# Optimization experiments

Measured on AMD Instinct MI355X. Metric: run time of the kernel, lower is better.

Reference implementation:

```python
import jax, jax.numpy as jnp
import numpy as np

EMBED = 1024
HEADS = 16
HEAD_DIM = EMBED // HEADS
FF = 4096
EPS = 1e-5


def layer_norm(x, g, b):
    mu = jnp.mean(x, axis=-1, keepdims=True)
    var = jnp.mean(jnp.square(x - mu), axis=-1, keepdims=True)
    return (x - mu) * jax.lax.rsqrt(var + EPS) * g + b


def setup_inputs() -> dict:
    key = jax.random.key(0)
    ks = jax.random.split(key, 16)
    s = 0.02
    x = jax.random.normal(ks[0], (4, 2048, EMBED), dtype=jnp.float32)
    d = {
        "x": x,
        "Wq": jax.random.normal(ks[1], (EMBED, EMBED), jnp.float32) * s,
        "bq": jnp.zeros((EMBED,), jnp.float32),
        "Wk": jax.random.normal(ks[2], (EMBED, EMBED), jnp.float32) * s,
        "bk": jnp.zeros((EMBED,), jnp.float32),
        "Wv": jax.random.normal(ks[3], (EMBED, EMBED), jnp.float32) * s,
        "bv": jnp.zeros((EMBED,), jnp.float32),
        "Wo": jax.random.normal(ks[4], (EMBED, EMBED), jnp.float32) * s,
        "bo": jnp.zeros((EMBED,), jnp.float32),
        "W1": jax.random.normal(ks[5], (EMBED, FF), jnp.float32) * s,
        "b1": jnp.zeros((FF,), jnp.float32),
        "W2": jax.random.normal(ks[6], (FF, EMBED), jnp.float32) * s,
        "b2": jnp.zeros((EMBED,), jnp.float32),
        "ln1_g": jnp.ones((EMBED,), jnp.float32),
        "ln1_b": jnp.zeros((EMBED,), jnp.float32),
        "ln2_g": jnp.ones((EMBED,), jnp.float32),
        "ln2_b": jnp.zeros((EMBED,), jnp.float32),
    }
    return d


def reference(x, Wq, bq, Wk, bk, Wv, bv, Wo, bo, W1, b1, W2, b2, ln1_g, ln1_b, ln2_g, ln2_b):
    B, S, E = x.shape
    scale = np.sqrt(HEAD_DIM).astype(np.float32)
    # project and split heads: (B, H, S, Dh)
    def heads(t):
        return t.reshape(B, S, HEADS, HEAD_DIM).transpose(0, 2, 1, 3)
    Q = heads(x @ Wq + bq)
    K = heads(x @ Wk + bk)
    V = heads(x @ Wv + bv)
    scores = jnp.einsum("bhqd,bhkd->bhqk", Q, K) / scale
    attn = jax.nn.softmax(scores, axis=-1)
    ctx = jnp.einsum("bhqk,bhkd->bhqd", attn, V)
    ctx = ctx.transpose(0, 2, 1, 3).reshape(B, S, E)
    attn_out = ctx @ Wo + bo
    x = layer_norm(x + attn_out, ln1_g, ln1_b)
    ff = jax.nn.relu(x @ W1 + b1) @ W2 + b2
    x = layer_norm(x + ff, ln2_g, ln2_b)
    return x
```

## Files before the change

kernel.cpp:

```cpp
#include <hip/hip_runtime.h>
#include <stdint.h>

typedef uint16_t u16;
typedef __bf16 bf16x8 __attribute__((ext_vector_type(8)));
typedef float f32x4 __attribute__((ext_vector_type(4)));

__device__ __forceinline__ float bf2f(u16 u) {
  union { uint32_t i; float f; } v; v.i = ((uint32_t)u) << 16; return v.f;
}
__device__ __forceinline__ u16 f2bf(float f) {
  union { float f; uint32_t i; } v; v.f = f;
  uint32_t r = v.i + 0x7fffu + ((v.i >> 16) & 1u);
  return (u16)(r >> 16);
}
__device__ __forceinline__ uint32_t pack2(float a, float b) {
  return (uint32_t)f2bf(a) | ((uint32_t)f2bf(b) << 16);
}
__device__ __forceinline__ void gll16(const u16* g, u16* l) {
  __builtin_amdgcn_global_load_lds((const __attribute__((address_space(1))) void*)g,
                                   (__attribute__((address_space(3))) void*)l, 16, 0, 0);
}

__global__ __launch_bounds__(256) void f32_to_bf16(
    const float* __restrict__ in, u16* __restrict__ out)
{
  int idx = blockIdx.x * 256 + threadIdx.x;
  float4 v = *(const float4*)(in + (size_t)idx * 4);
  uint2 o;
  o.x = pack2(v.x, v.y);
  o.y = pack2(v.z, v.w);
  *(uint2*)(out + (size_t)idx * 4) = o;
}

__global__ __launch_bounds__(256) void concat_bias(
    const float* __restrict__ a, const float* __restrict__ b,
    const float* __restrict__ c, float* __restrict__ o)
{
  int i = blockIdx.x * 256 + threadIdx.x;
  float v = (i < 1024) ? a[i] : ((i < 2048) ? b[i - 1024] : c[i - 2048]);
  o[i] = v;
}

__global__ __launch_bounds__(256) void transpose_f2b(
    const float* __restrict__ in, u16* __restrict__ out, int R, int C, int ldo)
{
  __shared__ u16 tile[32][33];
  int c0 = blockIdx.x * 32, r0 = blockIdx.y * 32;
  int x = threadIdx.x, y = threadIdx.y;
#pragma unroll
  for (int i = 0; i < 32; i += 8)
    tile[y + i][x] = f2bf(in[(size_t)(r0 + y + i) * C + (c0 + x)]);
  __syncthreads();
#pragma unroll
  for (int i = 0; i < 32; i += 8)
    out[(size_t)(c0 + y + i) * ldo + (r0 + x)] = tile[x][y + i];
}

__global__ __launch_bounds__(256) void transpose_v(
    const u16* __restrict__ src, u16* __restrict__ dst)
{
  __shared__ u16 tile[64][72];
  int kc = blockIdx.x;
  int bh = blockIdx.y;
  int b = bh >> 4, h = bh & 15;
  int t = threadIdx.x;
  int r = t >> 3;
  int c0 = (t & 7) * 8;
  const u16* s0 = src + ((size_t)(b * 2048 + kc * 64 + r) * 3072) + h * 64 + c0;
#pragma unroll
  for (int hh = 0; hh < 2; hh++)
    *(uint4*)(&tile[r + hh * 32][c0]) = *(const uint4*)(s0 + (size_t)hh * 32 * 3072);
  __syncthreads();
#pragma unroll
  for (int hh = 0; hh < 2; hh++) {
    int d = r + hh * 32;
    u16 vals[8];
#pragma unroll
    for (int p = 0; p < 8; p++) {
      int pos = c0 + p;
      int key = ((pos & 3) << 4) | ((pos >> 2) & 15);
      vals[p] = tile[key][d];
    }
    *(uint4*)(dst + ((size_t)bh * 64 + d) * 2048 + (size_t)kc * 64 + c0) = *(uint4*)vals;
  }
}

#define BM 128
#define BN 128
#define BK 64

__global__ __launch_bounds__(256, 2) void gemm_bt(
    const u16* __restrict__ A, const u16* __restrict__ BT,
    const float* __restrict__ bias, u16* __restrict__ C,
    int N, int K, int lda, int ldb, int ldc, int relu, int addC)
{
  __shared__ __align__(16) u16 As[BM][BK];
  __shared__ __align__(16) u16 Bs[BN][BK];
  int tid = threadIdx.x;
  int m0 = blockIdx.y * BM, n0 = blockIdx.x * BN;
  int wave = tid >> 6, lane = tid & 63;
  int quad = lane >> 4, tr = lane & 15;
  int wm = (wave >> 1) * 64, wn = (wave & 1) * 64;
  int tr7 = tr & 7;

  f32x4 zero = {0.f, 0.f, 0.f, 0.f};
  f32x4 acc[4][4];
#pragma unroll
  for (int i = 0; i < 4; i++)
#pragma unroll
    for (int j = 0; j < 4; j++) acc[i][j] = zero;

  int srow = tid >> 3;
  int sblk = (tid & 7) ^ (srow & 7);
  const u16* Abase = A  + (size_t)(m0 + srow) * lda + sblk * 8;
  const u16* Bbase = BT + (size_t)(n0 + srow) * ldb + sblk * 8;
  u16* la = &As[0][0] + tid * 8;
  u16* lb = &Bs[0][0] + tid * 8;

  for (int k0 = 0; k0 < K; k0 += BK) {
#pragma unroll
    for (int R = 0; R < 4; R++) {
      gll16(Abase + (size_t)(R * 32) * lda + k0, la + R * 2048);
      gll16(Bbase + (size_t)(R * 32) * ldb + k0, lb + R * 2048);
    }
    __syncthreads();
#pragma unroll
    for (int ks = 0; ks < 2; ks++) {
      bf16x8 af[4], bfr[4];
#pragma unroll
      for (int i = 0; i < 4; i++)
        af[i]  = *(const bf16x8*)(&As[wm + i*16 + tr][(((ks*4 + quad) ^ tr7)) * 8]);
#pragma unroll
      for (int j = 0; j < 4; j++)
        bfr[j] = *(const bf16x8*)(&Bs[wn + j*16 + tr][(((ks*4 + quad) ^ tr7)) * 8]);
#pragma unroll
      for (int i = 0; i < 4; i++)
#pragma unroll
        for (int j = 0; j < 4; j++)
          acc[i][j] = __builtin_amdgcn_mfma_f32_16x16x32_bf16(af[i], bfr[j], acc[i][j], 0, 0, 0);
    }
    __syncthreads();
  }

#pragma unroll
  for (int j = 0; j < 4; j++) {
    int n = n0 + wn + j*16 + tr;
    float bv = bias ? bias[n] : 0.f;
#pragma unroll
    for (int i = 0; i < 4; i++) {
      int mrow = m0 + wm + i*16 + quad*4;
#pragma unroll
      for (int r = 0; r < 4; r++) {
        size_t idx = (size_t)(mrow + r) * ldc + n;
        float v = acc[i][j][r] + bv;
        if (addC) v += bf2f(C[idx]);
        if (relu) v = v > 0.f ? v : 0.f;
        C[idx] = f2bf(v);
      }
    }
  }
}

__global__ __launch_bounds__(512, 4) void flash_attn(
    const u16* __restrict__ Qb, const u16* __restrict__ Kb,
    const u16* __restrict__ Vtg, u16* __restrict__ Ob, int ldqkv, int ldo)
{
  __shared__ __align__(16) u16 Ks[64][64];
  __shared__ __align__(16) u16 Vt[64][64];
  __shared__ __align__(16) u16 Ps[8][32][72];

  const int S = 2048;
  int tid = threadIdx.x;
  int wv = tid >> 6, lane = tid & 63;
  int quad = lane >> 4, tr = lane & 15;
  int tr7 = tr & 7;
  int bh = blockIdx.y;
  int b = bh >> 4, h = bh & 15;
  int q0 = blockIdx.x * 256;
  int wq = wv * 32;
  size_t rowbase = (size_t)b * S;
  int colbase = h * 64;

  bf16x8 qf[2][2];
#pragma unroll
  for (int i = 0; i < 2; i++)
#pragma unroll
    for (int ks = 0; ks < 2; ks++)
      qf[i][ks] = *(const bf16x8*)(Qb + (rowbase + q0 + wq + i*16 + tr) * ldqkv
                                   + colbase + ks*32 + quad*8);

  f32x4 zero = {0.f, 0.f, 0.f, 0.f};
  f32x4 o[2][4];
  float lsum[2][4];
#pragma unroll
  for (int i = 0; i < 2; i++)
#pragma unroll
    for (int r = 0; r < 4; r++) lsum[i][r] = 0.f;
#pragma unroll
  for (int i = 0; i < 2; i++)
#pragma unroll
    for (int j = 0; j < 4; j++) o[i][j] = zero;

  const float sc = 0.125f;

  int srow = tid >> 3;
  int sblk = (tid & 7) ^ (srow & 7);
  const u16* kgbase = Kb + (rowbase + srow) * ldqkv + colbase + sblk * 8;
  const u16* vgbase = Vtg + ((size_t)bh * 64 + srow) * 2048 + sblk * 8;
  u16* kl = &Ks[0][0] + tid * 8;
  u16* vl = &Vt[0][0] + tid * 8;

  for (int kv0 = 0; kv0 < S; kv0 += 64) {
    gll16(kgbase + (size_t)kv0 * ldqkv, kl);
    gll16(vgbase + kv0, vl);
    __syncthreads();

    f32x4 s[2][4];
#pragma unroll
    for (int i = 0; i < 2; i++)
#pragma unroll
      for (int j = 0; j < 4; j++) s[i][j] = zero;
#pragma unroll
    for (int ks = 0; ks < 2; ks++) {
      bf16x8 kf[4];
#pragma unroll
      for (int j = 0; j < 4; j++)
        kf[j] = *(const bf16x8*)(&Ks[j*16 + tr][((ks*4 + quad) ^ tr7) * 8]);
#pragma unroll
      for (int i = 0; i < 2; i++)
#pragma unroll
        for (int j = 0; j < 4; j++)
          s[i][j] = __builtin_amdgcn_mfma_f32_16x16x32_bf16(qf[i][ks], kf[j], s[i][j], 0, 0, 0);
    }

#pragma unroll
    for (int i = 0; i < 2; i++) {
#pragma unroll
      for (int r = 0; r < 4; r++) {
        float p0 = __expf(s[i][0][r] * sc);
        float p1 = __expf(s[i][1][r] * sc);
        float p2 = __expf(s[i][2][r] * sc);
        float p3 = __expf(s[i][3][r] * sc);
        lsum[i][r] += (p0 + p1) + (p2 + p3);
        uint2 w;
        w.x = (__float_as_uint(p0) >> 16) | (__float_as_uint(p1) & 0xffff0000u);
        w.y = (__float_as_uint(p2) >> 16) | (__float_as_uint(p3) & 0xffff0000u);
        *(uint2*)(&Ps[wv][i*16 + quad*4 + r][tr*4]) = w;
      }
    }

#pragma unroll
    for (int ks = 0; ks < 2; ks++) {
      bf16x8 pf[2];
#pragma unroll
      for (int i = 0; i < 2; i++)
        pf[i] = *(const bf16x8*)(&Ps[wv][i*16 + tr][ks*32 + quad*8]);
#pragma unroll
      for (int jd = 0; jd < 4; jd++) {
        bf16x8 vf = *(const bf16x8*)(&Vt[jd*16 + tr][((ks*4 + quad) ^ tr7) * 8]);
#pragma unroll
        for (int i = 0; i < 2; i++)
          o[i][jd] = __builtin_amdgcn_mfma_f32_16x16x32_bf16(pf[i], vf, o[i][jd], 0, 0, 0);
      }
    }
    __syncthreads();
  }

#pragma unroll
  for (int i = 0; i < 2; i++) {
#pragma unroll
    for (int r = 0; r < 4; r++) {
      float l = lsum[i][r];
      l += __shfl_xor(l, 1, 64);
      l += __shfl_xor(l, 2, 64);
      l += __shfl_xor(l, 4, 64);
      l += __shfl_xor(l, 8, 64);
      float inv = 1.f / l;
      size_t qrow = rowbase + q0 + wq + i*16 + quad*4 + r;
#pragma unroll
      for (int jd = 0; jd < 4; jd++)
        Ob[qrow * ldo + colbase + jd*16 + tr] = f2bf(o[i][jd][r] * inv);
    }
  }
}

__global__ __launch_bounds__(256) void add_ln_a(
    const float* __restrict__ X, const u16* __restrict__ Rr,
    const float* __restrict__ G, const float* __restrict__ Bb,
    u16* __restrict__ Y)
{
  int row = blockIdx.x;
  int tid = threadIdx.x;
  __shared__ float sbuf[4], qbuf[4];
  float4 xv = *(const float4*)(X + (size_t)row * 1024 + tid * 4);
  uint2 ru = *(const uint2*)(Rr + (size_t)row * 1024 + tid * 4);
  const u16* rs = (const u16*)&ru;
  const float* xs = (const float*)&xv;
  float v[4];
  float s = 0.f, q = 0.f;
#pragma unroll
  for (int e = 0; e < 4; e++) {
    float a = xs[e] + bf2f(rs[e]);
    v[e] = a; s += a; q += a * a;
  }
#pragma unroll
  for (int off = 1; off < 64; off <<= 1) {
    s += __shfl_xor(s, off, 64);
    q += __shfl_xor(q, off, 64);
  }
  if ((tid & 63) == 0) { sbuf[tid >> 6] = s; qbuf[tid >> 6] = q; }
  __syncthreads();
  s = sbuf[0] + sbuf[1] + sbuf[2] + sbuf[3];
  q = qbuf[0] + qbuf[1] + qbuf[2] + qbuf[3];
  float mu  = s * (1.f / 1024.f);
  float var = q * (1.f / 1024.f) - mu * mu;
  float inv = rsqrtf(var + 1e-5f);
#pragma unroll
  for (int e = 0; e < 4; e++) {
    int col = tid * 4 + e;
    float yv = (v[e] - mu) * inv * G[col] + Bb[col];
    Y[(size_t)row * 1024 + col] = f2bf(yv);
  }
}

__global__ __launch_bounds__(256) void add_ln_b(
    const u16* __restrict__ X, const u16* __restrict__ Rr,
    const float* __restrict__ G, const float* __restrict__ Bb,
    float* __restrict__ Y)
{
  int row = blockIdx.x;
  int tid = threadIdx.x;
  __shared__ float sbuf[4], qbuf[4];
  uint2 xu = *(const uint2*)(X  + (size_t)row * 1024 + tid * 4);
  uint2 ru = *(const uint2*)(Rr + (size_t)row * 1024 + tid * 4);
  const u16* xs = (const u16*)&xu;
  const u16* rs = (const u16*)&ru;
  float v[4];
  float s = 0.f, q = 0.f;
#pragma unroll
  for (int e = 0; e < 4; e++) {
    float a = bf2f(xs[e]) + bf2f(rs[e]);
    v[e] = a; s += a; q += a * a;
  }
#pragma unroll
  for (int off = 1; off < 64; off <<= 1) {
    s += __shfl_xor(s, off, 64);
    q += __shfl_xor(q, off, 64);
  }
  if ((tid & 63) == 0) { sbuf[tid >> 6] = s; qbuf[tid >> 6] = q; }
  __syncthreads();
  s = sbuf[0] + sbuf[1] + sbuf[2] + sbuf[3];
  q = qbuf[0] + qbuf[1] + qbuf[2] + qbuf[3];
  float mu  = s * (1.f / 1024.f);
  float var = q * (1.f / 1024.f) - mu * mu;
  float inv = rsqrtf(var + 1e-5f);
  float4 yv;
  float* yp = (float*)&yv;
#pragma unroll
  for (int e = 0; e < 4; e++) {
    int col = tid * 4 + e;
    yp[e] = (v[e] - mu) * inv * G[col] + Bb[col];
  }
  *(float4*)(Y + (size_t)row * 1024 + tid * 4) = yv;
}

extern "C" void kernel_launch(void* const* d_in, const int* in_sizes, int n_in,
                              void* d_out, int out_size, void* d_ws, size_t ws_size,
                              hipStream_t stream) {
  const float* x   = (const float*)d_in[0];
  const float* Wq  = (const float*)d_in[1];
  const float* bq  = (const float*)d_in[2];
  const float* Wk  = (const float*)d_in[3];
  const float* bk  = (const float*)d_in[4];
  const float* Wv  = (const float*)d_in[5];
  const float* bv  = (const float*)d_in[6];
  const float* Wo  = (const float*)d_in[7];
  const float* bo  = (const float*)d_in[8];
  const float* W1  = (const float*)d_in[9];
  const float* b1  = (const float*)d_in[10];
  const float* W2  = (const float*)d_in[11];
  const float* b2  = (const float*)d_in[12];
  const float* g1  = (const float*)d_in[13];
  const float* be1 = (const float*)d_in[14];
  const float* g2  = (const float*)d_in[15];
  const float* be2 = (const float*)d_in[16];
  float* out = (float*)d_out;
  u16* ws  = (u16*)d_ws;

  const int Nrow = 8192, E = 1024, FFd = 4096;
  const size_t M1 = 1048576;
  u16* xb     = ws;
  u16* WqkvT  = ws + 8  * M1;
  u16* WoT    = ws + 11 * M1;
  u16* W1T    = ws + 12 * M1;
  u16* W2T    = ws + 16 * M1;
  u16* QKV    = ws + 20 * M1;
  u16* Vtg    = ws;
  u16* X1     = ws;
  u16* F2     = ws + 20 * M1;
  float* bqkv = (float*)d_out;
  u16*  AO    = (u16*)d_out;
  u16*  Hc    = (u16*)d_out;

  dim3 tb(256);
  dim3 tt(32, 8);
  f32_to_bf16<<<dim3(8192), tb, 0, stream>>>(x, xb);
  transpose_f2b<<<dim3(E/32,  E/32),  tt, 0, stream>>>(Wq, WqkvT,        E,   E,   E);
  transpose_f2b<<<dim3(E/32,  E/32),  tt, 0, stream>>>(Wk, WqkvT + 1*M1, E,   E,   E);
  transpose_f2b<<<dim3(E/32,  E/32),  tt, 0, stream>>>(Wv, WqkvT + 2*M1, E,   E,   E);
  transpose_f2b<<<dim3(E/32,  E/32),  tt, 0, stream>>>(Wo, WoT,          E,   E,   E);
  transpose_f2b<<<dim3(FFd/32,E/32),  tt, 0, stream>>>(W1, W1T,          E,   FFd, E);
  transpose_f2b<<<dim3(E/32,  FFd/32),tt, 0, stream>>>(W2, W2T,          FFd, E,   FFd);
  concat_bias<<<dim3(12), tb, 0, stream>>>(bq, bk, bv, bqkv);

  gemm_bt<<<dim3(24, Nrow/BM), tb, 0, stream>>>(xb, WqkvT, bqkv, QKV,
                                                3072, E, E, E, 3072, 0, 0);
  transpose_v<<<dim3(32, 64), tb, 0, stream>>>(QKV + 2048, Vtg);
  flash_attn<<<dim3(8, 64), dim3(512), 0, stream>>>(QKV, QKV + 1024, Vtg,
                                                    QKV + 2048, 3072, 3072);
  gemm_bt<<<dim3(8, Nrow/BM), tb, 0, stream>>>(QKV + 2048, WoT, bo, AO,
                                               E, E, 3072, E, E, 0, 0);
  add_ln_a<<<dim3(Nrow), tb, 0, stream>>>(x, AO, g1, be1, X1);

  for (int c = 0; c < 2; c++) {
    gemm_bt<<<dim3(16, Nrow/BM), tb, 0, stream>>>(
        X1, W1T + (size_t)c * 2048 * E, b1 + c * 2048, Hc,
        2048, E, E, E, 2048, 1, 0);
    gemm_bt<<<dim3(8, Nrow/BM), tb, 0, stream>>>(
        Hc, W2T + (size_t)c * 2048, (c == 0 ? b2 : (const float*)nullptr), F2,
        E, 2048, 2048, FFd, E, 0, (c == 0 ? 0 : 1));
  }

  add_ln_b<<<dim3(Nrow), tb, 0, stream>>>(X1, F2, g2, be2, out);
}
```

Measured before the change: 533.9 us.

## Replace GEMM with triple-buffered 256x128 pipelined kernel using async LDS loads

Replaces the single-buffered 128x128 GEMM with a 512-thread, 256x128 tile kernel that keeps three LDS stages in flight via global_load_lds. It uses explicit vmcnt waits and one barrier per k-step instead of two syncthreads, and raises MFMA priority with setprio. The aim is to hide global-load latency behind MFMA work and raise reuse per tile. In exchange, LDS use grows to 144KB per block, which limits occupancy, and there are fewer blocks for the narrower GEMMs.

```diff
diff --git a/kernel.cpp b/kernel.cpp
--- a/kernel.cpp
+++ b/kernel.cpp
@@ -85,23 +85,23 @@
   }
 }
 
-#define BM 128
-#define BN 128
-#define BK 64
-
-__global__ __launch_bounds__(256, 2) void gemm_bt(
+#define GBM 256
+#define GBN 128
+#define GBK 64
+
+__global__ __launch_bounds__(512, 2) void gemm_pipe(
     const u16* __restrict__ A, const u16* __restrict__ BT,
     const float* __restrict__ bias, u16* __restrict__ C,
     int N, int K, int lda, int ldb, int ldc, int relu, int addC)
 {
-  __shared__ __align__(16) u16 As[BM][BK];
-  __shared__ __align__(16) u16 Bs[BN][BK];
+  __shared__ __align__(16) u16 As[3][GBM * GBK];
+  __shared__ __align__(16) u16 Bs[3][GBN * GBK];
   int tid = threadIdx.x;
-  int m0 = blockIdx.y * BM, n0 = blockIdx.x * BN;
+  int m0 = blockIdx.y * GBM, n0 = blockIdx.x * GBN;
   int wave = tid >> 6, lane = tid & 63;
-  int quad = lane >> 4, tr = lane & 15;
-  int wm = (wave >> 1) * 64, wn = (wave & 1) * 64;
-  int tr7 = tr & 7;
+  int quad = lane >> 4, tr = lane & 15, tr7 = tr & 7;
+  int wm = (wave >> 1) * 64;
+  int wn = (wave & 1) * 64;
 
   f32x4 zero = {0.f, 0.f, 0.f, 0.f};
   f32x4 acc[4][4];
@@ -112,43 +112,82 @@
 
   int srow = tid >> 3;
   int sblk = (tid & 7) ^ (srow & 7);
-  const u16* Abase = A  + (size_t)(m0 + srow) * lda + sblk * 8;
-  const u16* Bbase = BT + (size_t)(n0 + srow) * ldb + sblk * 8;
-  u16* la = &As[0][0] + tid * 8;
-  u16* lb = &Bs[0][0] + tid * 8;
-
-  for (int k0 = 0; k0 < K; k0 += BK) {
-#pragma unroll
-    for (int R = 0; R < 4; R++) {
-      gll16(Abase + (size_t)(R * 32) * lda + k0, la + R * 2048);
-      gll16(Bbase + (size_t)(R * 32) * ldb + k0, lb + R * 2048);
-    }
-    __syncthreads();
-#pragma unroll
-    for (int ks = 0; ks < 2; ks++) {
-      bf16x8 af[4], bfr[4];
+  const u16* gA = A  + (size_t)(m0 + srow) * lda + sblk * 8;
+  const u16* gB = BT + (size_t)(n0 + srow) * ldb + sblk * 8;
+  int l8 = tid * 8;
+  int NT = K >> 6;
+
+  u16 *a0 = As[0], *a1 = As[1], *a2 = As[2];
+  u16 *b0 = Bs[0], *b1 = Bs[1], *b2 = Bs[2];
+
+#define STAGE6(la, lb)                                                \
+  {                                                                   \
+    _Pragma("unroll")                                                 \
+    for (int R = 0; R < 4; R++)                                       \
+      gll16(gA + (size_t)(R * 64) * lda, (la) + l8 + R * 4096);       \
+    _Pragma("unroll")                                                 \
+    for (int R = 0; R < 2; R++)                                       \
+      gll16(gB + (size_t)(R * 64) * ldb, (lb) + l8 + R * 4096);       \
+    gA += GBK; gB += GBK;                                             \
+  }
+
+  STAGE6(a0, b0);
+  STAGE6(a1, b1);
+  asm volatile("s_waitcnt vmcnt(6)" ::: "memory");
+  __builtin_amdgcn_s_barrier();
+  __builtin_amdgcn_sched_barrier(0);
+
+  u16 *rA = a0, *nA = a1, *sA = a2;
+  u16 *rB = b0, *nB = b1, *sB = b2;
+
+  int aBase = (wm + tr) * GBK;
+  int bBase = (wn + tr) * GBK;
+  int kq0 = (quad ^ tr7) * 8;
+  int kq1 = ((4 + quad) ^ tr7) * 8;
+
+  for (int t = 0; t < NT; ++t) {
+    if (t + 2 < NT) STAGE6(sA, sB);
+    bf16x8 af[4][2], bfv[4][2];
+#pragma unroll
+    for (int i = 0; i < 4; i++) {
+      af[i][0] = *(const bf16x8*)(rA + aBase + i * 1024 + kq0);
+      af[i][1] = *(const bf16x8*)(rA + aBase + i * 1024 + kq1);
+    }
+#pragma unroll
+    for (int j = 0; j < 4; j++) {
+      bfv[j][0] = *(const bf16x8*)(rB + bBase + j * 1024 + kq0);
+      bfv[j][1] = *(const bf16x8*)(rB + bBase + j * 1024 + kq1);
+    }
+    __builtin_amdgcn_s_setprio(1);
+#pragma unroll
+    for (int ks = 0; ks < 2; ks++)
 #pragma unroll
       for (int i = 0; i < 4; i++)
-        af[i]  = *(const bf16x8*)(&As[wm + i*16 + tr][(((ks*4 + quad) ^ tr7)) * 8]);
-#pragma unroll
-      for (int j = 0; j < 4; j++)
-        bfr[j] = *(const bf16x8*)(&Bs[wn + j*16 + tr][(((ks*4 + quad) ^ tr7)) * 8]);
-#pragma unroll
-      for (int i = 0; i < 4; i++)
 #pragma unroll
         for (int j = 0; j < 4; j++)
-          acc[i][j] = __builtin_amdgcn_mfma_f32_16x16x32_bf16(af[i], bfr[j], acc[i][j], 0, 0, 0);
-    }
-    __syncthreads();
-  }
+          acc[i][j] = __builtin_amdgcn_mfma_f32_16x16x32_bf16(
+              af[i][ks], bfv[j][ks], acc[i][j], 0, 0, 0);
+    __builtin_amdgcn_s_setprio(0);
+
+    if (t + 1 < NT) {
+      if (t + 2 < NT) asm volatile("s_waitcnt vmcnt(6)" ::: "memory");
+      else            asm volatile("s_waitcnt vmcnt(0)" ::: "memory");
+      __builtin_amdgcn_s_barrier();
+      __builtin_amdgcn_sched_barrier(0);
+      u16* tp;
+      tp = rA; rA = nA; nA = sA; sA = tp;
+      tp = rB; rB = nB; nB = sB; sB = tp;
+    }
+  }
+#undef STAGE6
 
 #pragma unroll
   for (int j = 0; j < 4; j++) {
-    int n = n0 + wn + j*16 + tr;
+    int n = n0 + wn + j * 16 + tr;
     float bv = bias ? bias[n] : 0.f;
 #pragma unroll
     for (int i = 0; i < 4; i++) {
-      int mrow = m0 + wm + i*16 + quad*4;
+      int mrow = m0 + wm + i * 16 + quad * 4;
 #pragma unroll
       for (int r = 0; r < 4; r++) {
         size_t idx = (size_t)(mrow + r) * ldc + n;
@@ -404,6 +443,7 @@
 
   dim3 tb(256);
   dim3 tt(32, 8);
+  dim3 gb(512);
   f32_to_bf16<<<dim3(8192), tb, 0, stream>>>(x, xb);
   transpose_f2b<<<dim3(E/32,  E/32),  tt, 0, stream>>>(Wq, WqkvT,        E,   E,   E);
   transpose_f2b<<<dim3(E/32,  E/32),  tt, 0, stream>>>(Wk, WqkvT + 1*M1, E,   E,   E);
@@ -413,20 +453,20 @@
   transpose_f2b<<<dim3(E/32,  FFd/32),tt, 0, stream>>>(W2, W2T,          FFd, E,   FFd);
   concat_bias<<<dim3(12), tb, 0, stream>>>(bq, bk, bv, bqkv);
 
-  gemm_bt<<<dim3(24, Nrow/BM), tb, 0, stream>>>(xb, WqkvT, bqkv, QKV,
-                                                3072, E, E, E, 3072, 0, 0);
+  gemm_pipe<<<dim3(3072/GBN, Nrow/GBM), gb, 0, stream>>>(xb, WqkvT, bqkv, QKV,
+                                                         3072, E, E, E, 3072, 0, 0);
   transpose_v<<<dim3(32, 64), tb, 0, stream>>>(QKV + 2048, Vtg);
   flash_attn<<<dim3(8, 64), dim3(512), 0, stream>>>(QKV, QKV + 1024, Vtg,
                                                     QKV + 2048, 3072, 3072);
-  gemm_bt<<<dim3(8, Nrow/BM), tb, 0, stream>>>(QKV + 2048, WoT, bo, AO,
-                                               E, E, 3072, E, E, 0, 0);
+  gemm_pipe<<<dim3(E/GBN, Nrow/GBM), gb, 0, stream>>>(QKV + 2048, WoT, bo, AO,
+                                                      E, E, 3072, E, E, 0, 0);
   add_ln_a<<<dim3(Nrow), tb, 0, stream>>>(x, AO, g1, be1, X1);
 
   for (int c = 0; c < 2; c++) {
-    gemm_bt<<<dim3(16, Nrow/BM), tb, 0, stream>>>(
+    gemm_pipe<<<dim3(2048/GBN, Nrow/GBM), gb, 0, stream>>>(
         X1, W1T + (size_t)c * 2048 * E, b1 + c * 2048, Hc,
         2048, E, E, E, 2048, 1, 0);
-    gemm_bt<<<dim3(8, Nrow/BM), tb, 0, stream>>>(
+    gemm_pipe<<<dim3(E/GBN, Nrow/GBM), gb, 0, stream>>>(
         Hc, W2T + (size_t)c * 2048, (c == 0 ? b2 : (const float*)nullptr), F2,
         E, 2048, 2048, FFd, E, 0, (c == 0 ? 0 : 1));
   }
```

New measurement: 601.2 us. +12.6%, slower.

## Replace GEMM with 8-wave double-buffered ping-pong pipelined kernel

Applied to the files above, without the earlier changes.

Replaces the 128x128 single-buffered GEMM with a 512-thread kernel that uses 256-wide N tiles and 128 or 256 tall M tiles. It double-buffers LDS and interleaves global-to-LDS staging with MFMA quarter-blocks, using barriers, waitcnt control and setprio. The goal is to hide load latency behind compute and raise per-block reuse, where the old kernel stalled on each tile load. The cost is more LDS per block, hand-tuned waitcnt counts that are easy to get wrong, and fewer blocks in flight for the smaller GEMMs.

```diff
diff --git a/kernel.cpp b/kernel.cpp
--- a/kernel.cpp
+++ b/kernel.cpp
@@ -85,74 +85,157 @@
   }
 }
 
-#define BM 128
-#define BN 128
-#define BK 64
-
-__global__ __launch_bounds__(256, 2) void gemm_bt(
+
+#define BAR  __builtin_amdgcn_s_barrier()
+#define LGKM0 asm volatile("s_waitcnt lgkmcnt(0)" ::: "memory")
+#define SB0  __builtin_amdgcn_sched_barrier(0)
+
+template<int MFR>
+__global__ __launch_bounds__(512, 2) void gemm8p(
     const u16* __restrict__ A, const u16* __restrict__ BT,
     const float* __restrict__ bias, u16* __restrict__ C,
-    int N, int K, int lda, int ldb, int ldc, int relu, int addC)
-{
-  __shared__ __align__(16) u16 As[BM][BK];
-  __shared__ __align__(16) u16 Bs[BN][BK];
+    int K, int lda, int ldb, int ldc, int relu, int addC)
+{
+  constexpr int BM  = MFR * 32;
+  constexpr int MF2 = MFR / 2;
+  constexpr int GA  = BM / 64;
+  __shared__ __align__(16) u16 As[2][BM * 64];
+  __shared__ __align__(16) u16 Bs[2][256 * 64];
+
   int tid = threadIdx.x;
-  int m0 = blockIdx.y * BM, n0 = blockIdx.x * BN;
+  int m0 = blockIdx.y * BM, n0 = blockIdx.x * 256;
   int wave = tid >> 6, lane = tid & 63;
-  int quad = lane >> 4, tr = lane & 15;
-  int wm = (wave >> 1) * 64, wn = (wave & 1) * 64;
-  int tr7 = tr & 7;
+  int quad = lane >> 4, tr = lane & 15, tr7 = tr & 7;
+  int wm = (wave >> 2) * (BM / 2);
+  int wn = (wave & 3) * 64;
 
   f32x4 zero = {0.f, 0.f, 0.f, 0.f};
-  f32x4 acc[4][4];
-#pragma unroll
-  for (int i = 0; i < 4; i++)
-#pragma unroll
-    for (int j = 0; j < 4; j++) acc[i][j] = zero;
+  f32x4 acc[MFR][4];
+#pragma unroll
+  for (int f = 0; f < MFR; f++)
+#pragma unroll
+    for (int j = 0; j < 4; j++) acc[f][j] = zero;
 
   int srow = tid >> 3;
   int sblk = (tid & 7) ^ (srow & 7);
-  const u16* Abase = A  + (size_t)(m0 + srow) * lda + sblk * 8;
-  const u16* Bbase = BT + (size_t)(n0 + srow) * ldb + sblk * 8;
-  u16* la = &As[0][0] + tid * 8;
-  u16* lb = &Bs[0][0] + tid * 8;
-
-  for (int k0 = 0; k0 < K; k0 += BK) {
-#pragma unroll
-    for (int R = 0; R < 4; R++) {
-      gll16(Abase + (size_t)(R * 32) * lda + k0, la + R * 2048);
-      gll16(Bbase + (size_t)(R * 32) * ldb + k0, lb + R * 2048);
-    }
-    __syncthreads();
-#pragma unroll
-    for (int ks = 0; ks < 2; ks++) {
-      bf16x8 af[4], bfr[4];
-#pragma unroll
-      for (int i = 0; i < 4; i++)
-        af[i]  = *(const bf16x8*)(&As[wm + i*16 + tr][(((ks*4 + quad) ^ tr7)) * 8]);
-#pragma unroll
-      for (int j = 0; j < 4; j++)
-        bfr[j] = *(const bf16x8*)(&Bs[wn + j*16 + tr][(((ks*4 + quad) ^ tr7)) * 8]);
-#pragma unroll
-      for (int i = 0; i < 4; i++)
-#pragma unroll
-        for (int j = 0; j < 4; j++)
-          acc[i][j] = __builtin_amdgcn_mfma_f32_16x16x32_bf16(af[i], bfr[j], acc[i][j], 0, 0, 0);
-    }
-    __syncthreads();
-  }
+  const u16* gAs = A  + (size_t)(m0 + srow) * lda + sblk * 8;
+  const u16* gBs = BT + (size_t)(n0 + srow) * ldb + sblk * 8;
+  u16* lA0 = &As[0][0] + tid * 8;
+  u16* lA1 = &As[1][0] + tid * 8;
+  u16* lB0 = &Bs[0][0] + tid * 8;
+  u16* lB1 = &Bs[1][0] + tid * 8;
+
+  int aRow = (wm + tr) * 64;
+  int bRow = (wn + tr) * 64;
+  int kq0 = (quad ^ tr7) * 8;
+  int kq1 = ((4 + quad) ^ tr7) * 8;
+
+  int NT = K >> 6, NI = NT >> 1;
+
+#define STG_A(lbuf, h, T)                                                   \
+  { _Pragma("unroll")                                                       \
+    for (int g = (h) * (GA / 2); g < ((h) + 1) * (GA / 2); ++g)             \
+      gll16(gAs + (size_t)(T) * 64 + (size_t)(g * 64) * lda,                \
+            (lbuf) + g * 4096); }
+#define STG_B(lbuf, h, T)                                                   \
+  { _Pragma("unroll")                                                       \
+    for (int g = 2 * (h); g < 2 * (h) + 2; ++g)                             \
+      gll16(gBs + (size_t)(T) * 64 + (size_t)(g * 64) * ldb,                \
+            (lbuf) + g * 4096); }
+#define LD_A(buf, sub)                                                      \
+  { _Pragma("unroll")                                                       \
+    for (int f = 0; f < MF2; ++f) {                                         \
+      aq[f][0] = *(const bf16x8*)(&As[buf][aRow + ((sub) * MF2 + f) * 1024 + kq0]); \
+      aq[f][1] = *(const bf16x8*)(&As[buf][aRow + ((sub) * MF2 + f) * 1024 + kq1]); \
+    } }
+#define LD_B(buf, sub, dst)                                                 \
+  { _Pragma("unroll")                                                       \
+    for (int j = 0; j < 2; ++j) {                                           \
+      dst[j][0] = *(const bf16x8*)(&Bs[buf][bRow + ((sub) * 2 + j) * 1024 + kq0]); \
+      dst[j][1] = *(const bf16x8*)(&Bs[buf][bRow + ((sub) * 2 + j) * 1024 + kq1]); \
+    } }
+#define QUAD(msub, nsub, bsrc)                                              \
+  { _Pragma("unroll")                                                       \
+    for (int ks = 0; ks < 2; ++ks)                                          \
+      _Pragma("unroll")                                                     \
+      for (int f = 0; f < MF2; ++f)                                         \
+        _Pragma("unroll")                                                   \
+        for (int j = 0; j < 2; ++j)                                         \
+          acc[(msub) * MF2 + f][(nsub) * 2 + j] =                           \
+              __builtin_amdgcn_mfma_f32_16x16x32_bf16(                      \
+                  aq[f][ks], bsrc[j][ks],                                   \
+                  acc[(msub) * MF2 + f][(nsub) * 2 + j], 0, 0, 0); }
+
+  STG_A(lA0, 0, 0); STG_A(lA0, 1, 0);
+  STG_B(lB0, 0, 0); STG_B(lB0, 1, 0);
+  STG_B(lB1, 0, 1); STG_B(lB1, 1, 1);
+  asm volatile("s_waitcnt vmcnt(0)" ::: "memory");
+  BAR;
+
+  bf16x8 aq[MF2][2], bq0[2][2], bq1[2][2];
+
+  for (int i = 0; i < NI; ++i) {
+    int tb = 2 * i + 1, t2 = 2 * i + 2, t3 = 2 * i + 3;
+    bool more = (t2 < NT);
+    LD_A(0, 0); LD_B(0, 0, bq0);
+    STG_A(lA1, 0, tb);
+    BAR; LGKM0; SB0;
+    __builtin_amdgcn_s_setprio(1); QUAD(0, 0, bq0); __builtin_amdgcn_s_setprio(0);
+    BAR;
+    LD_B(0, 1, bq1);
+    STG_A(lA1, 1, tb);
+    BAR; LGKM0; SB0;
+    __builtin_amdgcn_s_setprio(1); QUAD(0, 1, bq1); __builtin_amdgcn_s_setprio(0);
+    BAR;
+    LD_A(0, 1);
+    if (more) STG_B(lB0, 0, t2);
+    BAR; LGKM0; SB0;
+    __builtin_amdgcn_s_setprio(1); QUAD(1, 1, bq1); __builtin_amdgcn_s_setprio(0);
+    BAR;
+    if (more) STG_B(lB0, 1, t2);
+    BAR;
+    __builtin_amdgcn_s_setprio(1); QUAD(1, 0, bq0); __builtin_amdgcn_s_setprio(0);
+    if (more) { asm volatile("s_waitcnt vmcnt(4)" ::: "memory"); }
+    else      { asm volatile("s_waitcnt vmcnt(0)" ::: "memory"); }
+    BAR;
+    LD_A(1, 0); LD_B(1, 0, bq0);
+    if (more) STG_A(lA0, 0, t2);
+    BAR; LGKM0; SB0;
+    __builtin_amdgcn_s_setprio(1); QUAD(0, 0, bq0); __builtin_amdgcn_s_setprio(0);
+    BAR;
+    LD_B(1, 1, bq1);
+    if (more) STG_A(lA0, 1, t2);
+    BAR; LGKM0; SB0;
+    __builtin_amdgcn_s_setprio(1); QUAD(0, 1, bq1); __builtin_amdgcn_s_setprio(0);
+    BAR;
+    LD_A(1, 1);
+    if (more) STG_B(lB1, 0, t3);
+    BAR; LGKM0; SB0;
+    __builtin_amdgcn_s_setprio(1); QUAD(1, 1, bq1); __builtin_amdgcn_s_setprio(0);
+    BAR;
+    if (more) STG_B(lB1, 1, t3);
+    BAR;
+    __builtin_amdgcn_s_setprio(1); QUAD(1, 0, bq0); __builtin_amdgcn_s_setprio(0);
+    if (more) { asm volatile("s_waitcnt vmcnt(4)" ::: "memory"); }
+    BAR;
+  }
+#undef STG_A
+#undef STG_B
+#undef LD_A
+#undef LD_B
+#undef QUAD
 
 #pragma unroll
   for (int j = 0; j < 4; j++) {
-    int n = n0 + wn + j*16 + tr;
+    int n = n0 + wn + j * 16 + tr;
     float bv = bias ? bias[n] : 0.f;
 #pragma unroll
-    for (int i = 0; i < 4; i++) {
-      int mrow = m0 + wm + i*16 + quad*4;
+    for (int f = 0; f < MFR; f++) {
+      int mrow = m0 + wm + f * 16 + quad * 4;
 #pragma unroll
       for (int r = 0; r < 4; r++) {
         size_t idx = (size_t)(mrow + r) * ldc + n;
-        float v = acc[i][j][r] + bv;
+        float v = acc[f][j][r] + bv;
         if (addC) v += bf2f(C[idx]);
         if (relu) v = v > 0.f ? v : 0.f;
         C[idx] = f2bf(v);
@@ -404,6 +487,7 @@
 
   dim3 tb(256);
   dim3 tt(32, 8);
+  dim3 gb(512);
   f32_to_bf16<<<dim3(8192), tb, 0, stream>>>(x, xb);
   transpose_f2b<<<dim3(E/32,  E/32),  tt, 0, stream>>>(Wq, WqkvT,        E,   E,   E);
   transpose_f2b<<<dim3(E/32,  E/32),  tt, 0, stream>>>(Wk, WqkvT + 1*M1, E,   E,   E);
@@ -413,22 +497,22 @@
   transpose_f2b<<<dim3(E/32,  FFd/32),tt, 0, stream>>>(W2, W2T,          FFd, E,   FFd);
   concat_bias<<<dim3(12), tb, 0, stream>>>(bq, bk, bv, bqkv);
 
-  gemm_bt<<<dim3(24, Nrow/BM), tb, 0, stream>>>(xb, WqkvT, bqkv, QKV,
-                                                3072, E, E, E, 3072, 0, 0);
+  gemm8p<8><<<dim3(3072/256, Nrow/256), gb, 0, stream>>>(xb, WqkvT, bqkv, QKV,
+                                                         E, E, E, 3072, 0, 0);
   transpose_v<<<dim3(32, 64), tb, 0, stream>>>(QKV + 2048, Vtg);
   flash_attn<<<dim3(8, 64), dim3(512), 0, stream>>>(QKV, QKV + 1024, Vtg,
                                                     QKV + 2048, 3072, 3072);
-  gemm_bt<<<dim3(8, Nrow/BM), tb, 0, stream>>>(QKV + 2048, WoT, bo, AO,
-                                               E, E, 3072, E, E, 0, 0);
+  gemm8p<4><<<dim3(E/256, Nrow/128), gb, 0, stream>>>(QKV + 2048, WoT, bo, AO,
+                                                      E, 3072, E, E, 0, 0);
   add_ln_a<<<dim3(Nrow), tb, 0, stream>>>(x, AO, g1, be1, X1);
 
   for (int c = 0; c < 2; c++) {
-    gemm_bt<<<dim3(16, Nrow/BM), tb, 0, stream>>>(
+    gemm8p<8><<<dim3(2048/256, Nrow/256), gb, 0, stream>>>(
         X1, W1T + (size_t)c * 2048 * E, b1 + c * 2048, Hc,
-        2048, E, E, E, 2048, 1, 0);
-    gemm_bt<<<dim3(8, Nrow/BM), tb, 0, stream>>>(
+        E, E, E, 2048, 1, 0);
+    gemm8p<4><<<dim3(E/256, Nrow/128), gb, 0, stream>>>(
         Hc, W2T + (size_t)c * 2048, (c == 0 ? b2 : (const float*)nullptr), F2,
-        E, 2048, 2048, FFd, E, 0, (c == 0 ? 0 : 1));
+        2048, 2048, FFd, E, 0, (c == 0 ? 0 : 1));
   }
 
   add_ln_b<<<dim3(Nrow), tb, 0, stream>>>(X1, F2, g2, be2, out);
```

Result: slower. 599.8 us (+12.3%).
